# Performance work log

Hardware: AMD Instinct MI355X
Metric: run time of the kernel (lower is better)

Reference implementation:

```python
import jax, jax.numpy as jnp
import numpy as np

B, V = 256, 128000


def setup_inputs() -> dict:
    key = jax.random.key(0)
    k1, k2 = jax.random.split(key)
    logits = jax.random.normal(k1, (B, V), dtype=jnp.float32)
    temperatures = jax.random.uniform(k2, (B,), dtype=jnp.float32)
    return {"logits": logits, "temperatures": temperatures}


def reference(logits, temperatures):
    # logits: (B, V) float32, temperatures: (B,) float32
    logits = logits.astype(jnp.float32)
    # greedy path (temperature == 0)
    greedy_tokens = jnp.argmax(logits, axis=-1)
    # temperature-scaled softmax; guard t==0 (torch divides by 0 -> nan probs,
    # but the final where() discards that lane, so safe-div is math-equivalent)
    t = temperatures[:, None]
    safe_t = jnp.where(t == 0.0, 1.0, t)
    probs = jax.nn.softmax(logits / safe_t, axis=-1)  # (B, V)
    # Gumbel-max trick as in torch: argmax(probs / Exp(1) noise)
    noise = jax.random.exponential(jax.random.key(1), probs.shape, dtype=jnp.float32)
    sample_tokens = jnp.argmax(probs / noise, axis=-1)
    return jnp.where(temperatures == 0.0, greedy_tokens, sample_tokens)
```

## Files before the change

### kernel.cpp

```cpp
#include <hip/hip_runtime.h>
#include <stdint.h>
#include <math.h>

constexpr int BROWS = 256;
constexpr int VCOLS = 128000;
constexpr int NQ    = 5;
constexpr int QCOLS = VCOLS / NQ;
constexpr int QV4   = QCOLS / 4;
constexpr int NBLK  = BROWS * NQ;
constexpr int NTHR  = 320;
constexpr int NITER = QV4 / (NTHR * 4);

__device__ __forceinline__ uint32_t fmap(float v) {
  uint32_t b = __float_as_uint(v);
  return b ^ (uint32_t)(((int32_t)b >> 31) | 0x80000000);
}
__device__ __forceinline__ float funmap(uint32_t s) {
  uint32_t b = s ^ (uint32_t)(((~(int32_t)s) >> 31) | 0x80000000);
  return __uint_as_float(b);
}

__device__ __forceinline__ unsigned long long mkkey(uint32_t s, int idx) {
  return ((unsigned long long)s << 32) | (uint32_t)(~(uint32_t)idx);
}

__device__ __forceinline__ uint32_t rotl(uint32_t x, uint32_t r) {
  return __builtin_amdgcn_alignbit(x, x, 32u - r);
}
__device__ __forceinline__ uint32_t tf_bits_x1(uint32_t x1i) {
  uint32_t x0 = 0u;
  uint32_t x1 = x1i;
#define R4(r0,r1,r2,r3) \
  x0 += x1; x1 = rotl(x1, r0); x1 ^= x0; \
  x0 += x1; x1 = rotl(x1, r1); x1 ^= x0; \
  x0 += x1; x1 = rotl(x1, r2); x1 ^= x0; \
  x0 += x1; x1 = rotl(x1, r3); x1 ^= x0;
  R4(13u,15u,26u,6u)
  x0 += 1u;            x1 += 0x1BD11BDBu + 1u;
  R4(17u,29u,16u,24u)
  x0 += 0x1BD11BDBu;   x1 += 0u + 2u;
  R4(13u,15u,26u,6u)
          x1 += 1u + 3u;
  R4(17u,29u,16u,24u)
  x0 += 1u;            x1 += 0x1BD11BDBu + 4u;
  R4(13u,15u,26u,6u)
  x0 += 0x1BD11BDBu;   x1 += 0u + 5u;
#undef R4
  return x0 ^ x1;
}

template <int NT>
__device__ __forceinline__ unsigned long long blockMaxU64(unsigned long long v) {
  __shared__ unsigned long long s_w[NT / 64];
  const int wid = threadIdx.x >> 6, lane = threadIdx.x & 63;
  #pragma unroll
  for (int off = 32; off > 0; off >>= 1) {
    unsigned long long o = __shfl_xor(v, off, 64);
    if (o > v) v = o;
  }
  if (lane == 0) s_w[wid] = v;
  __syncthreads();
  if (threadIdx.x == 0) {
    #pragma unroll
    for (int w = 1; w < NT / 64; ++w) if (s_w[w] > v) v = s_w[w];
    s_w[0] = v;
  }
  __syncthreads();
  return s_w[0];
}

extern "C" __global__ void __launch_bounds__(NTHR)
k1_rowmax(const float* __restrict__ logits,
          unsigned long long* __restrict__ partMax)
{
  const int blk = blockIdx.x;
  const int row = blk / NQ, q = blk % NQ;
  const float4* base =
      reinterpret_cast<const float4*>(logits + (size_t)row * VCOLS + q * QCOLS);
  const int idx0 = q * QCOLS;

  unsigned long long best = 0ull;
  for (int vv = threadIdx.x; vv < QV4; vv += NTHR) {
    float4 l4 = base[vv];
    int v0 = idx0 + vv * 4;
    unsigned long long k0 = mkkey(fmap(l4.x), v0 + 0);
    unsigned long long k1 = mkkey(fmap(l4.y), v0 + 1);
    unsigned long long k2 = mkkey(fmap(l4.z), v0 + 2);
    unsigned long long k3 = mkkey(fmap(l4.w), v0 + 3);
    if (k1 > k0) k0 = k1;
    if (k3 > k2) k2 = k3;
    if (k2 > k0) k0 = k2;
    if (k0 > best) best = k0;
  }
  best = blockMaxU64<NTHR>(best);
  if (threadIdx.x == 0) partMax[blk] = best;
}

extern "C" __global__ void __launch_bounds__(NTHR)
k2_sample(const float* __restrict__ logits,
          const float* __restrict__ temps,
          const unsigned long long* __restrict__ partMax,
          unsigned long long* __restrict__ sampPart)
{
  const int blk = blockIdx.x;
  const int row = blk / NQ, q = blk % NQ;
  const float4* base =
      reinterpret_cast<const float4*>(logits + (size_t)row * VCOLS + q * QCOLS);

  const float t = temps[row];
  const float safe_t = (t == 0.0f) ? 1.0f : t;
  const float inv_t = 1.0f / safe_t;

  unsigned long long pm = partMax[row * NQ];
  #pragma unroll
  for (int j = 1; j < NQ; ++j) {
    unsigned long long o = partMax[row * NQ + j];
    if (o > pm) pm = o;
  }
  const float M = funmap((uint32_t)(pm >> 32));

  const float c1 = inv_t * 1.4426950408889634f;
  const float c0 = fmaf(-M, c1, 0.5287663729448977f);

  const uint32_t rowbase = (uint32_t)row * (uint32_t)VCOLS;
  const uint32_t Ce = rowbase + (uint32_t)(q * QCOLS) + 1u;

  float bestv = -INFINITY;
  uint32_t bestx1 = 0u;

  #pragma unroll
  for (int it = 0; it < NITER; ++it) {
    const int vbase = it * (NTHR * 4) + (int)threadIdx.x;
    float4 L[4];
    #pragma unroll
    for (int u = 0; u < 4; ++u) L[u] = base[vbase + u * NTHR];

    #pragma unroll
    for (int u = 0; u < 4; ++u) {
      const uint32_t ce = Ce + (uint32_t)((vbase + u * NTHR) * 4);
      const float lx[4] = {L[u].x, L[u].y, L[u].z, L[u].w};
      #pragma unroll
      for (uint32_t k = 0; k < 4; ++k) {
        uint32_t x1i = ce + k;
        uint32_t bits = tf_bits_x1(x1i);
        float f = __uint_as_float((bits >> 9) | 0x3F800000u);
        float g = __builtin_amdgcn_logf(2.0f - f);
        float ln_noise2 = __builtin_amdgcn_logf(fabsf(g));
        float val = fmaf(lx[k], c1, c0) - ln_noise2;
        if (val > bestv) { bestv = val; bestx1 = x1i; }
      }
    }
  }

  const int colidx = (int)(bestx1 - 1u - rowbase);
  unsigned long long best = mkkey(fmap(bestv), colidx);
  best = blockMaxU64<NTHR>(best);
  if (threadIdx.x == 0) sampPart[blk] = best;
}

extern "C" __global__ void __launch_bounds__(BROWS)
k3_final(const float* __restrict__ temps,
         const unsigned long long* __restrict__ partMax,
         const unsigned long long* __restrict__ sampPart,
         int* __restrict__ out)
{
  const int r = threadIdx.x;
  if (r >= BROWS) return;
  unsigned long long g = partMax[r * NQ];
  unsigned long long s = sampPart[r * NQ];
  #pragma unroll
  for (int j = 1; j < NQ; ++j) {
    unsigned long long og = partMax[r * NQ + j];
    unsigned long long os = sampPart[r * NQ + j];
    if (og > g) g = og;
    if (os > s) s = os;
  }
  const int greedy = (int)(~(uint32_t)g);
  const int samp   = (int)(~(uint32_t)s);
  out[r] = (temps[r] == 0.0f) ? greedy : samp;
}

extern "C" void kernel_launch(void* const* d_in, const int* in_sizes, int n_in,
                              void* d_out, int out_size, void* d_ws, size_t ws_size,
                              hipStream_t stream) {
  const float* logits = (const float*)d_in[0];
  const float* temps  = (const float*)d_in[1];
  int* out = (int*)d_out;

  unsigned long long* partMax  = (unsigned long long*)d_ws;
  unsigned long long* sampPart = partMax + NBLK;

  k1_rowmax<<<NBLK, NTHR, 0, stream>>>(logits, partMax);
  k2_sample<<<NBLK, NTHR, 0, stream>>>(logits, temps, partMax, sampPart);
  k3_final<<<1, BROWS, 0, stream>>>(temps, partMax, sampPart, out);
}
```

Measured before the change: 97.03 us.

## Fuse rowmax into sampling kernel, drop max subtraction, prefetch and interleave Threefry

Merges the separate row-max pass into the sampling kernel, so logits are read once and the greedy argmax is computed alongside the Gumbel-max argmax. The softmax max offset and constant are dropped because argmax is invariant to a per-row shift. The main loop now double-buffers the next float4 loads with unroll 1, and four Threefry streams are interleaved for more instruction-level parallelism. This removes one full pass over the 131MB logits plus a kernel launch. The cost is higher register pressure, and the fp32 shift change could alter rounding and flip near-ties.

```diff
diff --git a/kernel.cpp b/kernel.cpp
--- a/kernel.cpp
+++ b/kernel.cpp
@@ -15,10 +15,6 @@
   uint32_t b = __float_as_uint(v);
   return b ^ (uint32_t)(((int32_t)b >> 31) | 0x80000000);
 }
-__device__ __forceinline__ float funmap(uint32_t s) {
-  uint32_t b = s ^ (uint32_t)(((~(int32_t)s) >> 31) | 0x80000000);
-  return __uint_as_float(b);
-}
 
 __device__ __forceinline__ unsigned long long mkkey(uint32_t s, int idx) {
   return ((unsigned long long)s << 32) | (uint32_t)(~(uint32_t)idx);
@@ -27,26 +23,36 @@
 __device__ __forceinline__ uint32_t rotl(uint32_t x, uint32_t r) {
   return __builtin_amdgcn_alignbit(x, x, 32u - r);
 }
-__device__ __forceinline__ uint32_t tf_bits_x1(uint32_t x1i) {
-  uint32_t x0 = 0u;
-  uint32_t x1 = x1i;
-#define R4(r0,r1,r2,r3) \
-  x0 += x1; x1 = rotl(x1, r0); x1 ^= x0; \
-  x0 += x1; x1 = rotl(x1, r1); x1 ^= x0; \
-  x0 += x1; x1 = rotl(x1, r2); x1 ^= x0; \
-  x0 += x1; x1 = rotl(x1, r3); x1 ^= x0;
-  R4(13u,15u,26u,6u)
-  x0 += 1u;            x1 += 0x1BD11BDBu + 1u;
-  R4(17u,29u,16u,24u)
-  x0 += 0x1BD11BDBu;   x1 += 0u + 2u;
-  R4(13u,15u,26u,6u)
-          x1 += 1u + 3u;
-  R4(17u,29u,16u,24u)
-  x0 += 1u;            x1 += 0x1BD11BDBu + 4u;
-  R4(13u,15u,26u,6u)
-  x0 += 0x1BD11BDBu;   x1 += 0u + 5u;
-#undef R4
-  return x0 ^ x1;
+
+__device__ __forceinline__ void tf4_bits(uint32_t i0, uint32_t i1, uint32_t i2,
+                                         uint32_t i3, uint32_t o[4]) {
+  uint32_t a0, a1, a2, a3;
+  uint32_t b0 = i0, b1 = i1, b2 = i2, b3 = i3;
+#define RND(r) \
+  a0 += b0; b0 = rotl(b0, r) ^ a0; \
+  a1 += b1; b1 = rotl(b1, r) ^ a1; \
+  a2 += b2; b2 = rotl(b2, r) ^ a2; \
+  a3 += b3; b3 = rotl(b3, r) ^ a3;
+  a0 = b0; b0 = rotl(b0, 13u) ^ a0;
+  a1 = b1; b1 = rotl(b1, 13u) ^ a1;
+  a2 = b2; b2 = rotl(b2, 13u) ^ a2;
+  a3 = b3; b3 = rotl(b3, 13u) ^ a3;
+  RND(15u) RND(26u) RND(6u)
+  a0 += 1u; a1 += 1u; a2 += 1u; a3 += 1u;
+  b0 += 0x1BD11BDCu; b1 += 0x1BD11BDCu; b2 += 0x1BD11BDCu; b3 += 0x1BD11BDCu;
+  RND(17u) RND(29u) RND(16u) RND(24u)
+  a0 += 0x1BD11BDBu; a1 += 0x1BD11BDBu; a2 += 0x1BD11BDBu; a3 += 0x1BD11BDBu;
+  b0 += 2u; b1 += 2u; b2 += 2u; b3 += 2u;
+  RND(13u) RND(15u) RND(26u) RND(6u)
+  b0 += 4u; b1 += 4u; b2 += 4u; b3 += 4u;
+  RND(17u) RND(29u) RND(16u) RND(24u)
+  a0 += 1u; a1 += 1u; a2 += 1u; a3 += 1u;
+  b0 += 0x1BD11BDFu; b1 += 0x1BD11BDFu; b2 += 0x1BD11BDFu; b3 += 0x1BD11BDFu;
+  RND(13u) RND(15u) RND(26u) RND(6u)
+  a0 += 0x1BD11BDBu; a1 += 0x1BD11BDBu; a2 += 0x1BD11BDBu; a3 += 0x1BD11BDBu;
+  b0 += 5u; b1 += 5u; b2 += 5u; b3 += 5u;
+#undef RND
+  o[0] = a0 ^ b0; o[1] = a1 ^ b1; o[2] = a2 ^ b2; o[3] = a3 ^ b3;
 }
 
 template <int NT>
@@ -70,37 +76,10 @@
 }
 
 extern "C" __global__ void __launch_bounds__(NTHR)
-k1_rowmax(const float* __restrict__ logits,
-          unsigned long long* __restrict__ partMax)
-{
-  const int blk = blockIdx.x;
-  const int row = blk / NQ, q = blk % NQ;
-  const float4* base =
-      reinterpret_cast<const float4*>(logits + (size_t)row * VCOLS + q * QCOLS);
-  const int idx0 = q * QCOLS;
-
-  unsigned long long best = 0ull;
-  for (int vv = threadIdx.x; vv < QV4; vv += NTHR) {
-    float4 l4 = base[vv];
-    int v0 = idx0 + vv * 4;
-    unsigned long long k0 = mkkey(fmap(l4.x), v0 + 0);
-    unsigned long long k1 = mkkey(fmap(l4.y), v0 + 1);
-    unsigned long long k2 = mkkey(fmap(l4.z), v0 + 2);
-    unsigned long long k3 = mkkey(fmap(l4.w), v0 + 3);
-    if (k1 > k0) k0 = k1;
-    if (k3 > k2) k2 = k3;
-    if (k2 > k0) k0 = k2;
-    if (k0 > best) best = k0;
-  }
-  best = blockMaxU64<NTHR>(best);
-  if (threadIdx.x == 0) partMax[blk] = best;
-}
-
-extern "C" __global__ void __launch_bounds__(NTHR)
-k2_sample(const float* __restrict__ logits,
-          const float* __restrict__ temps,
-          const unsigned long long* __restrict__ partMax,
-          unsigned long long* __restrict__ sampPart)
+k_main(const float* __restrict__ logits,
+       const float* __restrict__ temps,
+       unsigned long long* __restrict__ gPart,
+       unsigned long long* __restrict__ sPart)
 {
   const int blk = blockIdx.x;
   const int row = blk / NQ, q = blk % NQ;
@@ -109,69 +88,71 @@
 
   const float t = temps[row];
   const float safe_t = (t == 0.0f) ? 1.0f : t;
-  const float inv_t = 1.0f / safe_t;
-
-  unsigned long long pm = partMax[row * NQ];
-  #pragma unroll
-  for (int j = 1; j < NQ; ++j) {
-    unsigned long long o = partMax[row * NQ + j];
-    if (o > pm) pm = o;
-  }
-  const float M = funmap((uint32_t)(pm >> 32));
-
-  const float c1 = inv_t * 1.4426950408889634f;
-  const float c0 = fmaf(-M, c1, 0.5287663729448977f);
+  const float c1 = (1.0f / safe_t) * 1.4426950408889634f;
 
   const uint32_t rowbase = (uint32_t)row * (uint32_t)VCOLS;
   const uint32_t Ce = rowbase + (uint32_t)(q * QCOLS) + 1u;
 
-  float bestv = -INFINITY;
-  uint32_t bestx1 = 0u;
+  float gv = -INFINITY; uint32_t gx = 0u;
+  float bv = -INFINITY; uint32_t bx = 0u;
 
-  #pragma unroll
+  int vb = (int)threadIdx.x;
+  float4 A0 = base[vb], A1 = base[vb + NTHR],
+         A2 = base[vb + 2 * NTHR], A3 = base[vb + 3 * NTHR];
+
+  #pragma unroll 1
   for (int it = 0; it < NITER; ++it) {
-    const int vbase = it * (NTHR * 4) + (int)threadIdx.x;
-    float4 L[4];
-    #pragma unroll
-    for (int u = 0; u < 4; ++u) L[u] = base[vbase + u * NTHR];
+    const int nvb = vb + 4 * NTHR;
+    float4 B0, B1, B2, B3;
+    if (it + 1 < NITER) {
+      B0 = base[nvb]; B1 = base[nvb + NTHR];
+      B2 = base[nvb + 2 * NTHR]; B3 = base[nvb + 3 * NTHR];
+    }
 
+    const float4 As[4] = {A0, A1, A2, A3};
     #pragma unroll
     for (int u = 0; u < 4; ++u) {
-      const uint32_t ce = Ce + (uint32_t)((vbase + u * NTHR) * 4);
-      const float lx[4] = {L[u].x, L[u].y, L[u].z, L[u].w};
+      const uint32_t ce = Ce + (uint32_t)((vb + u * NTHR) * 4);
+      const float lx[4] = {As[u].x, As[u].y, As[u].z, As[u].w};
+      uint32_t bits[4];
+      tf4_bits(ce, ce + 1u, ce + 2u, ce + 3u, bits);
       #pragma unroll
       for (uint32_t k = 0; k < 4; ++k) {
-        uint32_t x1i = ce + k;
-        uint32_t bits = tf_bits_x1(x1i);
-        float f = __uint_as_float((bits >> 9) | 0x3F800000u);
+        const uint32_t x1i = ce + k;
+        float f = __uint_as_float((bits[k] >> 9) | 0x3F800000u);
         float g = __builtin_amdgcn_logf(2.0f - f);
-        float ln_noise2 = __builtin_amdgcn_logf(fabsf(g));
-        float val = fmaf(lx[k], c1, c0) - ln_noise2;
-        if (val > bestv) { bestv = val; bestx1 = x1i; }
+        float g2 = __builtin_amdgcn_logf(fabsf(g));
+        float val = fmaf(lx[k], c1, -g2);
+        if (lx[k] > gv) { gv = lx[k]; gx = x1i; }
+        if (val  > bv) { bv = val;    bx = x1i; }
       }
     }
+
+    vb = nvb;
+    A0 = B0; A1 = B1; A2 = B2; A3 = B3;
   }
 
-  const int colidx = (int)(bestx1 - 1u - rowbase);
-  unsigned long long best = mkkey(fmap(bestv), colidx);
-  best = blockMaxU64<NTHR>(best);
-  if (threadIdx.x == 0) sampPart[blk] = best;
+  const int gcol = (int)(gx - 1u - rowbase);
+  const int scol = (int)(bx - 1u - rowbase);
+  unsigned long long gk = blockMaxU64<NTHR>(mkkey(fmap(gv), gcol));
+  unsigned long long sk = blockMaxU64<NTHR>(mkkey(fmap(bv), scol));
+  if (threadIdx.x == 0) { gPart[blk] = gk; sPart[blk] = sk; }
 }
 
 extern "C" __global__ void __launch_bounds__(BROWS)
 k3_final(const float* __restrict__ temps,
-         const unsigned long long* __restrict__ partMax,
-         const unsigned long long* __restrict__ sampPart,
+         const unsigned long long* __restrict__ gPart,
+         const unsigned long long* __restrict__ sPart,
          int* __restrict__ out)
 {
   const int r = threadIdx.x;
   if (r >= BROWS) return;
-  unsigned long long g = partMax[r * NQ];
-  unsigned long long s = sampPart[r * NQ];
+  unsigned long long g = gPart[r * NQ];
+  unsigned long long s = sPart[r * NQ];
   #pragma unroll
   for (int j = 1; j < NQ; ++j) {
-    unsigned long long og = partMax[r * NQ + j];
-    unsigned long long os = sampPart[r * NQ + j];
+    unsigned long long og = gPart[r * NQ + j];
+    unsigned long long os = sPart[r * NQ + j];
     if (og > g) g = og;
     if (os > s) s = os;
   }
@@ -187,10 +168,9 @@
   const float* temps  = (const float*)d_in[1];
   int* out = (int*)d_out;
 
-  unsigned long long* partMax  = (unsigned long long*)d_ws;
-  unsigned long long* sampPart = partMax + NBLK;
+  unsigned long long* gPart = (unsigned long long*)d_ws;
+  unsigned long long* sPart = gPart + NBLK;
 
-  k1_rowmax<<<NBLK, NTHR, 0, stream>>>(logits, partMax);
-  k2_sample<<<NBLK, NTHR, 0, stream>>>(logits, temps, partMax, sampPart);
-  k3_final<<<1, BROWS, 0, stream>>>(temps, partMax, sampPart, out);
+  k_main<<<NBLK, NTHR, 0, stream>>>(logits, temps, gPart, sPart);
+  k3_final<<<1, BROWS, 0, stream>>>(temps, gPart, sPart, out);
 }
```

After: 81.72 us. 1.19x faster.
